# Optimization experiments

Measured on AMD Instinct MI355X. Metric: run time of the kernel, lower is better.

Reference implementation:

```python
import jax, jax.numpy as jnp
import numpy as np

N = 100000
E = 1600000
IN, HID, MID, OUT = 128, 64, 32, 1
EPS = 1e-5


def setup_inputs() -> dict:
    key = jax.random.key(0)
    ks = jax.random.split(key, 12)
    inp = {
        "x": jax.random.normal(ks[0], (N, IN), dtype=jnp.float32),
        "edge_index": jax.random.randint(ks[1], (2, E), 0, N, dtype=jnp.int32),
        # GCN layer 1
        "W1": jax.random.normal(ks[2], (IN, HID), dtype=jnp.float32) / np.sqrt(IN),
        "b1": jnp.zeros((HID,), dtype=jnp.float32),
        "g1": jax.random.uniform(ks[3], (HID,), dtype=jnp.float32, minval=0.5, maxval=1.5),
        "be1": jax.random.normal(ks[4], (HID,), dtype=jnp.float32) * 0.1,
        "m1": jax.random.normal(ks[5], (HID,), dtype=jnp.float32) * 0.1,
        "v1": jax.random.uniform(ks[6], (HID,), dtype=jnp.float32, minval=0.5, maxval=1.5),
        # GCN layer 2
        "W2": jax.random.normal(ks[7], (HID, HID), dtype=jnp.float32) / np.sqrt(HID),
        "b2": jnp.zeros((HID,), dtype=jnp.float32),
        "g2": jax.random.uniform(ks[8], (HID,), dtype=jnp.float32, minval=0.5, maxval=1.5),
        "be2": jax.random.normal(ks[9], (HID,), dtype=jnp.float32) * 0.1,
        "m2": jax.random.normal(ks[10], (HID,), dtype=jnp.float32) * 0.1,
        "v2": jax.random.uniform(ks[11], (HID,), dtype=jnp.float32, minval=0.5, maxval=1.5),
    }
    kc = jax.random.split(jax.random.key(1), 2)
    inp["Wc1"] = jax.random.normal(kc[0], (HID, MID), dtype=jnp.float32) / np.sqrt(HID)
    inp["bc1"] = jnp.zeros((MID,), dtype=jnp.float32)
    inp["Wc2"] = jax.random.normal(kc[1], (MID, OUT), dtype=jnp.float32) / np.sqrt(MID)
    inp["bc2"] = jnp.zeros((OUT,), dtype=jnp.float32)
    return inp


def _gcn_layer(x, W, b, src, dst, n):
    # PyG GCNConv: h = X W; add self-loops; sym-normalize; scatter-add; + bias
    h = x @ W                                               # [N, F]
    deg = jax.ops.segment_sum(jnp.ones((src.shape[0],), h.dtype), dst,
                              num_segments=n) + 1.0          # self-loop adds 1
    dinv = jax.lax.rsqrt(deg)                               # deg >= 1 always
    norm = dinv[src] * dinv[dst]                            # [E]
    agg = jax.ops.segment_sum(norm[:, None] * h[src], dst, num_segments=n)
    agg = agg + (dinv * dinv)[:, None] * h                  # self-loop term
    return agg + b


def _bn_eval(x, g, b, m, v):
    return (x - m) * jax.lax.rsqrt(v + EPS) * g + b


def reference(x, edge_index, W1, b1, g1, be1, m1, v1,
              W2, b2, g2, be2, m2, v2, Wc1, bc1, Wc2, bc2):
    src, dst = edge_index[0], edge_index[1]
    n = x.shape[0]
    h = jax.nn.relu(_bn_eval(_gcn_layer(x, W1, b1, src, dst, n), g1, be1, m1, v1))
    h = jax.nn.relu(_bn_eval(_gcn_layer(h, W2, b2, src, dst, n), g2, be2, m2, v2))
    h = jax.nn.relu(h @ Wc1 + bc1)
    out = h @ Wc2 + bc2                                      # [N, 1]
    return jax.nn.sigmoid(out).squeeze(-1)                   # [N]
```

## Files before the change

kernel.cpp:

```cpp
#include <hip/hip_runtime.h>
#include <math.h>

#define EPSV 1e-5f
#define SBLK 512
#define WNODES 256

typedef _Float16 h16;
typedef _Float16 half8 __attribute__((ext_vector_type(8)));
typedef float f32x4 __attribute__((ext_vector_type(4)));

static __device__ __forceinline__ float h2f(unsigned int u16) {
  unsigned short s = (unsigned short)u16;
  h16 h;
  __builtin_memcpy(&h, &s, 2);
  return (float)h;
}

__global__ __launch_bounds__(256) void k_cnt(const int* __restrict__ ei,
                                             int* __restrict__ cnt512, int E, int nw) {
  __shared__ int hist[512];
  int s = blockIdx.x;
  for (int i = threadIdx.x; i < nw; i += 256) hist[i] = 0;
  __syncthreads();
  long long elo = (long long)s * E / SBLK, ehi = (long long)(s + 1) * E / SBLK;
  for (long long i = elo + threadIdx.x; i < ehi; i += 256)
    atomicAdd(&hist[ei[E + i] >> 8], 1);
  __syncthreads();
  for (int i = threadIdx.x; i < nw; i += 256) cnt512[s * nw + i] = hist[i];
}

__global__ __launch_bounds__(512) void k_scan2(int* __restrict__ cnt512,
                                               int* __restrict__ woffs, int E, int nw) {
  int w = threadIdx.x;
  int tot = 0;
  if (w < nw) {
#pragma unroll 8
    for (int s = 0; s < SBLK; ++s) tot += cnt512[s * nw + w];
  }
  __shared__ int sh[512];
  sh[w] = tot;
  __syncthreads();
  for (int off = 1; off < 512; off <<= 1) {
    int u = (w >= off) ? sh[w - off] : 0;
    __syncthreads();
    sh[w] += u;
    __syncthreads();
  }
  int base = sh[w] - tot;
  if (w < nw) {
    woffs[w] = base;
    int run = base;
    for (int s = 0; s < SBLK; ++s) {
      int c = cnt512[s * nw + w];
      cnt512[s * nw + w] = run;
      run += c;
    }
  }
  if (w == 0) woffs[nw] = E;
}

__global__ __launch_bounds__(256) void k_append(const int* __restrict__ ei,
                                                const int* __restrict__ base512,
                                                int* __restrict__ bucket, int E, int nw) {
  __shared__ int cur[512];
  int s = blockIdx.x;
  for (int i = threadIdx.x; i < nw; i += 256) cur[i] = base512[s * nw + i];
  __syncthreads();
  long long elo = (long long)s * E / SBLK, ehi = (long long)(s + 1) * E / SBLK;
  for (long long i = elo + threadIdx.x; i < ehi; i += 256) {
    int d = ei[E + i];
    int src = ei[i];
    int pos = atomicAdd(&cur[d >> 8], 1);
    bucket[pos] = src | ((d & 255) << 24);
  }
}

__global__ __launch_bounds__(256) void k_sortw(const int* __restrict__ bucket,
                                               const int* __restrict__ woffs,
                                               int* __restrict__ csr,
                                               int* __restrict__ offs,
                                               float* __restrict__ dinv, int N, int E) {
  __shared__ int cnt[WNODES];
  __shared__ int sc[WNODES];
  __shared__ int cur[WNODES];
  int w = blockIdx.x, t = threadIdx.x;
  int lo = woffs[w], hi = woffs[w + 1];
  cnt[t] = 0;
  __syncthreads();
  for (int i = lo + t; i < hi; i += 256)
    atomicAdd(&cnt[((unsigned)bucket[i]) >> 24], 1);
  __syncthreads();
  int c = cnt[t];
  sc[t] = c;
  __syncthreads();
  for (int off = 1; off < 256; off <<= 1) {
    int u = (t >= off) ? sc[t - off] : 0;
    __syncthreads();
    sc[t] += u;
    __syncthreads();
  }
  int excl = sc[t] - c;
  int node = w * WNODES + t;
  if (node < N) {
    offs[node] = lo + excl;
    dinv[node] = rsqrtf((float)c + 1.f);
  }
  cur[t] = excl;
  if (w == 0 && t == 0) offs[N] = E;
  __syncthreads();
  for (int i = lo + t; i < hi; i += 256) {
    unsigned p = (unsigned)bucket[i];
    int pos = atomicAdd(&cur[p >> 24], 1);
    csr[lo + pos] = (int)(p & 0xFFFFFFu);
  }
}

__global__ __launch_bounds__(256, 1) void k_gemm1(const float* __restrict__ x,
                                                  const float* __restrict__ W,
                                                  h16* __restrict__ h, int N) {
  int lane = threadIdx.x & 63;
  int wave = threadIdx.x >> 6;
  int q = lane >> 4, r16 = lane & 15;
  half8 bf[4][4];
#pragma unroll
  for (int t = 0; t < 4; ++t)
#pragma unroll
    for (int s = 0; s < 4; ++s) {
      const float* wp = W + (s * 32 + q * 8) * 64 + t * 16 + r16;
#pragma unroll
      for (int j = 0; j < 8; ++j) bf[t][s][j] = (h16)wp[j * 64];
    }
  long long base_row = (long long)blockIdx.x * 128 + wave * 32;
#pragma unroll
  for (int rt = 0; rt < 2; ++rt) {
    long long row0 = base_row + rt * 16;
    long long arow = row0 + r16;
    if (arow >= N) arow = N - 1;
    const float* xp = x + arow * 128 + q * 8;
    half8 af[4];
#pragma unroll
    for (int s = 0; s < 4; ++s) {
      float4 v0 = *(const float4*)(xp + s * 32);
      float4 v1 = *(const float4*)(xp + s * 32 + 4);
      af[s][0] = (h16)v0.x; af[s][1] = (h16)v0.y;
      af[s][2] = (h16)v0.z; af[s][3] = (h16)v0.w;
      af[s][4] = (h16)v1.x; af[s][5] = (h16)v1.y;
      af[s][6] = (h16)v1.z; af[s][7] = (h16)v1.w;
    }
    f32x4 acc[4] = {{0.f, 0.f, 0.f, 0.f}, {0.f, 0.f, 0.f, 0.f},
                    {0.f, 0.f, 0.f, 0.f}, {0.f, 0.f, 0.f, 0.f}};
#pragma unroll
    for (int s = 0; s < 4; ++s)
#pragma unroll
      for (int t = 0; t < 4; ++t)
        acc[t] = __builtin_amdgcn_mfma_f32_16x16x32_f16(af[s], bf[t][s], acc[t], 0, 0, 0);
#pragma unroll
    for (int t = 0; t < 4; ++t)
#pragma unroll
      for (int rr = 0; rr < 4; ++rr) {
        long long row = row0 + q * 4 + rr;
        if (row < N) h[row * 64 + t * 16 + r16] = (h16)acc[t][rr];
      }
  }
}

__global__ __launch_bounds__(256, 1) void k_gemm2(const h16* __restrict__ xh,
                                                  const float* __restrict__ W,
                                                  h16* __restrict__ h, int N) {
  int lane = threadIdx.x & 63;
  int wave = threadIdx.x >> 6;
  int q = lane >> 4, r16 = lane & 15;
  half8 bf[4][2];
#pragma unroll
  for (int t = 0; t < 4; ++t)
#pragma unroll
    for (int s = 0; s < 2; ++s) {
      const float* wp = W + (s * 32 + q * 8) * 64 + t * 16 + r16;
#pragma unroll
      for (int j = 0; j < 8; ++j) bf[t][s][j] = (h16)wp[j * 64];
    }
  long long base_row = (long long)blockIdx.x * 128 + wave * 32;
#pragma unroll
  for (int rt = 0; rt < 2; ++rt) {
    long long row0 = base_row + rt * 16;
    long long arow = row0 + r16;
    if (arow >= N) arow = N - 1;
    half8 af[2];
#pragma unroll
    for (int s = 0; s < 2; ++s)
      af[s] = *(const half8*)(xh + arow * 64 + s * 32 + q * 8);
    f32x4 acc[4] = {{0.f, 0.f, 0.f, 0.f}, {0.f, 0.f, 0.f, 0.f},
                    {0.f, 0.f, 0.f, 0.f}, {0.f, 0.f, 0.f, 0.f}};
#pragma unroll
    for (int s = 0; s < 2; ++s)
#pragma unroll
      for (int t = 0; t < 4; ++t)
        acc[t] = __builtin_amdgcn_mfma_f32_16x16x32_f16(af[s], bf[t][s], acc[t], 0, 0, 0);
#pragma unroll
    for (int t = 0; t < 4; ++t)
#pragma unroll
      for (int rr = 0; rr < 4; ++rr) {
        long long row = row0 + q * 4 + rr;
        if (row < N) h[row * 64 + t * 16 + r16] = (h16)acc[t][rr];
      }
  }
}

__global__ __launch_bounds__(256) void k_gath(const int* __restrict__ csr,
                                              const int* __restrict__ offs,
                                              const float* __restrict__ dinv,
                                              const h16* __restrict__ hin,
                                              const float* __restrict__ b,
                                              const float* __restrict__ g,
                                              const float* __restrict__ be,
                                              const float* __restrict__ m,
                                              const float* __restrict__ v,
                                              h16* __restrict__ hout, int N) {
  int lane = threadIdx.x & 63;
  int node = (int)(((long long)blockIdx.x * blockDim.x + threadIdx.x) >> 6);
  if (node >= N) return;
  node = __builtin_amdgcn_readfirstlane(node);
  int beg = offs[node], end = offs[node + 1];
  float acc = 0.f;
  int j = beg;
  for (; j + 4 <= end; j += 4) {
    int s0 = csr[j], s1 = csr[j + 1], s2 = csr[j + 2], s3 = csr[j + 3];
    float w0 = dinv[s0], w1 = dinv[s1], w2 = dinv[s2], w3 = dinv[s3];
    float h0 = (float)hin[(long long)s0 * 64 + lane];
    float h1 = (float)hin[(long long)s1 * 64 + lane];
    float h2 = (float)hin[(long long)s2 * 64 + lane];
    float h3 = (float)hin[(long long)s3 * 64 + lane];
    acc = fmaf(w0, h0, acc);
    acc = fmaf(w1, h1, acc);
    acc = fmaf(w2, h2, acc);
    acc = fmaf(w3, h3, acc);
  }
  for (; j < end; ++j) {
    int s = csr[j];
    acc = fmaf(dinv[s], (float)hin[(long long)s * 64 + lane], acc);
  }
  float di = dinv[node];
  acc = fmaf(di, (float)hin[(long long)node * 64 + lane], acc);
  acc = fmaf(di, acc, b[lane]);
  float A = g[lane] * rsqrtf(v[lane] + EPSV);
  float B = be[lane] - m[lane] * A;
  hout[(long long)node * 64 + lane] = (h16)fmaxf(fmaf(acc, A, B), 0.f);
}

__global__ __launch_bounds__(256) void k_cls(const h16* __restrict__ h,
                                             const float* __restrict__ Wc1,
                                             const float* __restrict__ bc1,
                                             const float* __restrict__ Wc2,
                                             const float* __restrict__ bc2,
                                             float* __restrict__ out, int N) {
  __shared__ float sW1[64 * 32];
  __shared__ float sW2[32];
  __shared__ float sb1[32];
  for (int i = threadIdx.x; i < 64 * 32; i += blockDim.x) sW1[i] = Wc1[i];
  if (threadIdx.x < 32) {
    sW2[threadIdx.x] = Wc2[threadIdx.x];
    sb1[threadIdx.x] = bc1[threadIdx.x];
  }
  __syncthreads();
  int node = blockIdx.x * blockDim.x + threadIdx.x;
  if (node >= N) return;
  const uint4* hp = (const uint4*)(h + (long long)node * 64);
  float mid[32];
#pragma unroll
  for (int j = 0; j < 32; ++j) mid[j] = sb1[j];
#pragma unroll
  for (int j4 = 0; j4 < 8; ++j4) {
    uint4 qv = hp[j4];
    unsigned int pk[4] = {qv.x, qv.y, qv.z, qv.w};
#pragma unroll
    for (int c = 0; c < 4; ++c) {
      float f0 = h2f(pk[c] & 0xffffu);
      float f1 = h2f(pk[c] >> 16);
      int f = j4 * 8 + c * 2;
#pragma unroll
      for (int j = 0; j < 32; ++j) mid[j] = fmaf(f0, sW1[f * 32 + j], mid[j]);
#pragma unroll
      for (int j = 0; j < 32; ++j) mid[j] = fmaf(f1, sW1[(f + 1) * 32 + j], mid[j]);
    }
  }
  float o = bc2[0];
#pragma unroll
  for (int j = 0; j < 32; ++j) o = fmaf(fmaxf(mid[j], 0.f), sW2[j], o);
  out[node] = 1.f / (1.f + expf(-o));
}

extern "C" void kernel_launch(void* const* d_in, const int* in_sizes, int n_in,
                              void* d_out, int out_size, void* d_ws, size_t ws_size,
                              hipStream_t stream) {
  const float* x  = (const float*)d_in[0];
  const int* ei   = (const int*)d_in[1];
  const float* W1 = (const float*)d_in[2];
  const float* b1 = (const float*)d_in[3];
  const float* g1 = (const float*)d_in[4];
  const float* be1 = (const float*)d_in[5];
  const float* m1 = (const float*)d_in[6];
  const float* v1 = (const float*)d_in[7];
  const float* W2 = (const float*)d_in[8];
  const float* b2 = (const float*)d_in[9];
  const float* g2 = (const float*)d_in[10];
  const float* be2 = (const float*)d_in[11];
  const float* m2 = (const float*)d_in[12];
  const float* v2 = (const float*)d_in[13];
  const float* Wc1 = (const float*)d_in[14];
  const float* bc1 = (const float*)d_in[15];
  const float* Wc2 = (const float*)d_in[16];
  const float* bc2 = (const float*)d_in[17];
  float* out = (float*)d_out;

  int N = in_sizes[0] / 128;
  int E = in_sizes[1] / 2;
  int Npad = ((N + 63) / 64) * 64;
  int nw = (N + WNODES - 1) / WNODES;

  char* ws = (char*)d_ws;
  h16*   bufA   = (h16*)ws;
  h16*   bufB   = bufA + (long long)N * 64;
  int*   bucket = (int*)(bufB + (long long)N * 64);
  int*   csr    = bucket + E;
  int*   cnt512 = csr + E;
  int*   woffs  = cnt512 + SBLK * nw;
  int*   offs   = woffs + nw + 64;
  float* dinv   = (float*)(offs + Npad + 64);
  size_t need = (size_t)((char*)(dinv + Npad) - (char*)d_ws);
  if (need > ws_size) return;

  k_cnt<<<SBLK, 256, 0, stream>>>(ei, cnt512, E, nw);
  k_scan2<<<1, 512, 0, stream>>>(cnt512, woffs, E, nw);
  k_append<<<SBLK, 256, 0, stream>>>(ei, cnt512, bucket, E, nw);
  k_sortw<<<nw, 256, 0, stream>>>(bucket, woffs, csr, offs, dinv, N, E);

  k_gemm1<<<(N + 127) / 128, 256, 0, stream>>>(x, W1, bufA, N);
  k_gath<<<(N * 64 + 255) / 256, 256, 0, stream>>>(csr, offs, dinv, bufA,
                                                   b1, g1, be1, m1, v1, bufB, N);
  k_gemm2<<<(N + 127) / 128, 256, 0, stream>>>(bufB, W2, bufA, N);
  k_gath<<<(N * 64 + 255) / 256, 256, 0, stream>>>(csr, offs, dinv, bufA,
                                                   b2, g2, be2, m2, v2, bufB, N);
  k_cls<<<(N + 255) / 256, 256, 0, stream>>>(bufB, Wc1, bc1, Wc2, bc2, out, N);
}
```

Measured before the change: 372.3 us.

## Split single-block bucket scan into per-bucket parallel scan and unroll gather by eight

New measurement: 320.7 us. 13.9% less time.

```diff
diff --git a/kernel.cpp b/kernel.cpp
--- a/kernel.cpp
+++ b/kernel.cpp
@@ -29,42 +29,48 @@
   for (int i = threadIdx.x; i < nw; i += 256) cnt512[s * nw + i] = hist[i];
 }
 
-__global__ __launch_bounds__(512) void k_scan2(int* __restrict__ cnt512,
-                                               int* __restrict__ woffs, int E, int nw) {
-  int w = threadIdx.x;
-  int tot = 0;
-  if (w < nw) {
-#pragma unroll 8
-    for (int s = 0; s < SBLK; ++s) tot += cnt512[s * nw + w];
-  }
-  __shared__ int sh[512];
-  sh[w] = tot;
+__global__ __launch_bounds__(512) void k_scanA(int* __restrict__ cnt512,
+                                               int* __restrict__ wtot, int nw) {
+  int w = blockIdx.x, t = threadIdx.x;
+  int c = cnt512[t * nw + w];
+  __shared__ int sc[512];
+  sc[t] = c;
   __syncthreads();
   for (int off = 1; off < 512; off <<= 1) {
-    int u = (w >= off) ? sh[w - off] : 0;
-    __syncthreads();
-    sh[w] += u;
-    __syncthreads();
-  }
-  int base = sh[w] - tot;
-  if (w < nw) {
-    woffs[w] = base;
-    int run = base;
-    for (int s = 0; s < SBLK; ++s) {
-      int c = cnt512[s * nw + w];
-      cnt512[s * nw + w] = run;
-      run += c;
-    }
-  }
-  if (w == 0) woffs[nw] = E;
+    int u = (t >= off) ? sc[t - off] : 0;
+    __syncthreads();
+    sc[t] += u;
+    __syncthreads();
+  }
+  cnt512[t * nw + w] = sc[t] - c;
+  if (t == 511) wtot[w] = sc[511];
+}
+
+__global__ __launch_bounds__(512) void k_scanB(const int* __restrict__ wtot,
+                                               int* __restrict__ woffs, int nw, int E) {
+  int t = threadIdx.x;
+  int c = (t < nw) ? wtot[t] : 0;
+  __shared__ int sc[512];
+  sc[t] = c;
+  __syncthreads();
+  for (int off = 1; off < 512; off <<= 1) {
+    int u = (t >= off) ? sc[t - off] : 0;
+    __syncthreads();
+    sc[t] += u;
+    __syncthreads();
+  }
+  if (t < nw) woffs[t] = sc[t] - c;
+  if (t == 0) woffs[nw] = E;
 }
 
 __global__ __launch_bounds__(256) void k_append(const int* __restrict__ ei,
                                                 const int* __restrict__ base512,
+                                                const int* __restrict__ woffs,
                                                 int* __restrict__ bucket, int E, int nw) {
   __shared__ int cur[512];
   int s = blockIdx.x;
-  for (int i = threadIdx.x; i < nw; i += 256) cur[i] = base512[s * nw + i];
+  for (int i = threadIdx.x; i < nw; i += 256)
+    cur[i] = base512[s * nw + i] + woffs[i];
   __syncthreads();
   long long elo = (long long)s * E / SBLK, ehi = (long long)(s + 1) * E / SBLK;
   for (long long i = elo + threadIdx.x; i < ehi; i += 256) {
@@ -223,17 +229,27 @@
   int beg = offs[node], end = offs[node + 1];
   float acc = 0.f;
   int j = beg;
-  for (; j + 4 <= end; j += 4) {
-    int s0 = csr[j], s1 = csr[j + 1], s2 = csr[j + 2], s3 = csr[j + 3];
+  for (; j + 8 <= end; j += 8) {
+    int s0 = csr[j],     s1 = csr[j + 1], s2 = csr[j + 2], s3 = csr[j + 3];
+    int s4 = csr[j + 4], s5 = csr[j + 5], s6 = csr[j + 6], s7 = csr[j + 7];
     float w0 = dinv[s0], w1 = dinv[s1], w2 = dinv[s2], w3 = dinv[s3];
+    float w4 = dinv[s4], w5 = dinv[s5], w6 = dinv[s6], w7 = dinv[s7];
     float h0 = (float)hin[(long long)s0 * 64 + lane];
     float h1 = (float)hin[(long long)s1 * 64 + lane];
     float h2 = (float)hin[(long long)s2 * 64 + lane];
     float h3 = (float)hin[(long long)s3 * 64 + lane];
+    float h4 = (float)hin[(long long)s4 * 64 + lane];
+    float h5 = (float)hin[(long long)s5 * 64 + lane];
+    float h6 = (float)hin[(long long)s6 * 64 + lane];
+    float h7 = (float)hin[(long long)s7 * 64 + lane];
     acc = fmaf(w0, h0, acc);
     acc = fmaf(w1, h1, acc);
     acc = fmaf(w2, h2, acc);
     acc = fmaf(w3, h3, acc);
+    acc = fmaf(w4, h4, acc);
+    acc = fmaf(w5, h5, acc);
+    acc = fmaf(w6, h6, acc);
+    acc = fmaf(w7, h7, acc);
   }
   for (; j < end; ++j) {
     int s = csr[j];
@@ -323,15 +339,17 @@
   int*   bucket = (int*)(bufB + (long long)N * 64);
   int*   csr    = bucket + E;
   int*   cnt512 = csr + E;
-  int*   woffs  = cnt512 + SBLK * nw;
+  int*   wtot   = cnt512 + SBLK * nw;
+  int*   woffs  = wtot + 512;
   int*   offs   = woffs + nw + 64;
   float* dinv   = (float*)(offs + Npad + 64);
   size_t need = (size_t)((char*)(dinv + Npad) - (char*)d_ws);
   if (need > ws_size) return;
 
   k_cnt<<<SBLK, 256, 0, stream>>>(ei, cnt512, E, nw);
-  k_scan2<<<1, 512, 0, stream>>>(cnt512, woffs, E, nw);
-  k_append<<<SBLK, 256, 0, stream>>>(ei, cnt512, bucket, E, nw);
+  k_scanA<<<nw, 512, 0, stream>>>(cnt512, wtot, nw);
+  k_scanB<<<1, 512, 0, stream>>>(wtot, woffs, nw, E);
+  k_append<<<SBLK, 256, 0, stream>>>(ei, cnt512, woffs, bucket, E, nw);
   k_sortw<<<nw, 256, 0, stream>>>(bucket, woffs, csr, offs, dinv, N, E);
 
   k_gemm1<<<(N + 127) / 128, 256, 0, stream>>>(x, W1, bufA, N);
```
